# Kernel tuning notes

Hardware: AMD Instinct MI355X
Metric: run time of the kernel (lower is better)

Reference implementation:

```python
import jax, jax.numpy as jnp
import numpy as np

EMBED = 1024
HEADS = 16
HEAD_DIM = EMBED // HEADS
B, S = 4, 2048


def setup_inputs() -> dict:
    key = jax.random.key(0)
    ks = jax.random.split(key, 8)
    values = jax.random.normal(ks[0], (B, S, EMBED), dtype=jnp.float32)
    keys_in = jax.random.normal(ks[1], (B, S, EMBED), dtype=jnp.float32)
    query = jax.random.normal(ks[2], (B, S, EMBED), dtype=jnp.float32)
    mask = jnp.ones((B, 1, 1, S), dtype=jnp.int32)
    sc = 1.0 / np.sqrt(HEAD_DIM)
    Wv = jax.random.normal(ks[3], (HEAD_DIM, HEAD_DIM), dtype=jnp.float32) * sc
    Wk = jax.random.normal(ks[4], (HEAD_DIM, HEAD_DIM), dtype=jnp.float32) * sc
    Wq = jax.random.normal(ks[5], (HEAD_DIM, HEAD_DIM), dtype=jnp.float32) * sc
    Wo = jax.random.normal(ks[6], (EMBED, EMBED), dtype=jnp.float32) * (1.0 / np.sqrt(EMBED))
    bo = jnp.zeros((EMBED,), dtype=jnp.float32)
    return {"values": values, "keys": keys_in, "query": query, "mask": mask,
            "Wv": Wv, "Wk": Wk, "Wq": Wq, "Wo": Wo, "bo": bo}


def reference(values, keys, query, mask, Wv, Wk, Wq, Wo, bo):
    n = query.shape[0]
    vl, kl, ql = values.shape[1], keys.shape[1], query.shape[1]
    h, d = HEADS, HEAD_DIM
    # split heads: [n, len, h, d]
    v = values.reshape(n, vl, h, d)
    k = keys.reshape(n, kl, h, d)
    q = query.reshape(n, ql, h, d)
    # per-head linear projections (torch Linear: x @ W.T), shared across heads
    v = jnp.einsum('nlhd,ed->nlhe', v, Wv)
    k = jnp.einsum('nlhd,ed->nlhe', k, Wk)
    q = jnp.einsum('nlhd,ed->nlhe', q, Wq)
    # attention scores [n, h, q, k]
    energy = jnp.einsum('nqhd,nkhd->nhqk', q, k)
    energy = jnp.where(mask == 0, jnp.float32(-1e20), energy)
    # NOTE: original scales by sqrt(embed_size), not sqrt(head_dim)
    attn = jax.nn.softmax(energy / jnp.sqrt(jnp.float32(EMBED)), axis=3)
    out = jnp.einsum('nhql,nlhd->nqhd', attn, v).reshape(n, ql, h * d)
    return out @ Wo.T + bo
```

## Files before the change

### kernel.cpp

```cpp
#include <hip/hip_runtime.h>
#include <hip/hip_bf16.h>


#define SS 2048
#define HH 16
#define DD 64

typedef __attribute__((ext_vector_type(8))) short bf16x8;
typedef __attribute__((ext_vector_type(4))) short s16x4;
typedef __attribute__((ext_vector_type(4))) float f32x4;
typedef __attribute__((ext_vector_type(16))) float f32x16;

__device__ __forceinline__ short f2bf(float f) {
  union { float f; unsigned u; } c; c.f = f;
  unsigned r = (c.u + 0x7FFFu + ((c.u >> 16) & 1u)) >> 16;
  return (short)r;
}

__device__ __forceinline__ int cvtpk(float lo, float hi) {
  int r;
  asm("v_cvt_pk_bf16_f32 %0, %1, %2" : "=v"(r) : "v"(lo), "v"(hi));
  return r;
}

__device__ __forceinline__ float fexp2(float x) {
  float r;
  asm("v_exp_f32 %0, %1" : "=v"(r) : "v"(x));
  return r;
}

__global__ __launch_bounds__(256) void proj_kernel(
    const float* __restrict__ xq, const float* __restrict__ xk, const float* __restrict__ xv,
    const float* __restrict__ Wq, const float* __restrict__ Wk, const float* __restrict__ Wv,
    short* __restrict__ qp, short* __restrict__ kp, short* __restrict__ vp)
{
  __shared__ short xlds[128][72];
  __shared__ short wlds[3][64][72];
  const int t = threadIdx.x;
  const int lane = t & 63;
  const int w = t >> 6;
  const int l15 = lane & 15, l4 = lane >> 4;

  const float* wsrc[3] = {Wq, Wk, Wv};
#pragma unroll
  for (int z = 0; z < 3; ++z) {
#pragma unroll
    for (int i = 0; i < 4; ++i) {
      int fi = (t + i * 256) * 4;
      int row = fi >> 6, col = fi & 63;
      float4 a = *(const float4*)(wsrc[z] + fi);
      s16x4 sv = { f2bf(a.x), f2bf(a.y), f2bf(a.z), f2bf(a.w) };
      *(s16x4*)&wlds[z][row][col] = sv;
    }
  }

  const long r0 = (long)blockIdx.x * 128;
  const float* xin[3] = {xq, xk, xv};
  short* outp[3] = {qp, kp, vp};
  const float SCQ = 0.03125f * 1.4426950408889634f;

#pragma unroll
  for (int z = 0; z < 3; ++z) {
    __syncthreads();
    const float* src = xin[z] + r0 * 64;
#pragma unroll
    for (int i = 0; i < 8; ++i) {
      int fi = (t + i * 256) * 4;
      int row = fi >> 6, col = fi & 63;
      float4 a = *(const float4*)(src + fi);
      s16x4 sv = { f2bf(a.x), f2bf(a.y), f2bf(a.z), f2bf(a.w) };
      *(s16x4*)&xlds[row][col] = sv;
    }
    __syncthreads();

    bf16x8 af[2][2];
#pragma unroll
    for (int mi = 0; mi < 2; ++mi)
#pragma unroll
      for (int kb = 0; kb < 2; ++kb)
        af[mi][kb] = *(const bf16x8*)&xlds[w * 32 + mi * 16 + l15][kb * 32 + l4 * 8];

    f32x4 acc[2][4];
#pragma unroll
    for (int mi = 0; mi < 2; ++mi)
#pragma unroll
      for (int nt = 0; nt < 4; ++nt)
        acc[mi][nt] = (f32x4){0.f, 0.f, 0.f, 0.f};

#pragma unroll
    for (int nt = 0; nt < 4; ++nt)
#pragma unroll
      for (int kb = 0; kb < 2; ++kb) {
        bf16x8 bfr = *(const bf16x8*)&wlds[z][nt * 16 + l15][kb * 32 + l4 * 8];
#pragma unroll
        for (int mi = 0; mi < 2; ++mi)
          acc[mi][nt] = __builtin_amdgcn_mfma_f32_16x16x32_bf16(af[mi][kb], bfr, acc[mi][nt], 0, 0, 0);
      }

    short* dst = outp[z];
    const float sc = (z == 0) ? SCQ : 1.0f;
#pragma unroll
    for (int mi = 0; mi < 2; ++mi)
#pragma unroll
      for (int nt = 0; nt < 4; ++nt)
#pragma unroll
        for (int j = 0; j < 4; ++j) {
          int r = (int)r0 + w * 32 + mi * 16 + l4 * 4 + j;
          int e = nt * 16 + l15;
          int h = r & 15, bs = r >> 4;
          int b = bs >> 11, s = bs & 2047;
          dst[(((long)(b * 16 + h) * 2048 + s) << 6) + e] = f2bf(acc[mi][nt][j] * sc);
        }
  }
}

__global__ __launch_bounds__(256) void wo_cvt(const float* __restrict__ Wo,
                                              short* __restrict__ wob) {
  long i = ((long)blockIdx.x * 256 + threadIdx.x) * 4;
  float4 a = *(const float4*)(Wo + i);
  s16x4 sv = { f2bf(a.x), f2bf(a.y), f2bf(a.z), f2bf(a.w) };
  *(s16x4*)(wob + i) = sv;
}

__global__ __launch_bounds__(256) void vt_kernel(const short* __restrict__ vp,
                                                 short* __restrict__ vpt) {
  __shared__ short tl[64][72];
  const int t = threadIdx.x;
  const long base_in = (long)blockIdx.y * SS * DD + (long)blockIdx.x * 64 * DD;
#pragma unroll
  for (int i = 0; i < 2; ++i) {
    int c = t + i * 256;
    int s = c >> 3, d0 = (c & 7) * 8;
    bf16x8 v = *(const bf16x8*)(vp + base_in + s * 64 + d0);
#pragma unroll
    for (int j = 0; j < 8; ++j) tl[d0 + j][s] = v[j];
  }
  __syncthreads();
  const long base_out = (long)blockIdx.y * DD * SS + (long)blockIdx.x * 64;
#pragma unroll
  for (int i = 0; i < 2; ++i) {
    int c = t + i * 256;
    int d = c >> 3, s0 = (c & 7) * 8;
    *(bf16x8*)(vpt + base_out + (long)d * SS + s0) = *(const bf16x8*)&tl[d][s0];
  }
}

__global__ __launch_bounds__(256, 4) void attn_kernel(
    const short* __restrict__ qp, const short* __restrict__ kp, const short* __restrict__ vpt,
    const int* __restrict__ mask, short* __restrict__ ao)
{
  __shared__ short klds[64][72];
  __shared__ short vtlds[64][72];
  __shared__ int tile_ok[32];
  const int t = threadIdx.x, lane = t & 63, w = t >> 6;
  const int l31 = lane & 31, hi = lane >> 5;
  const int wg = (blockIdx.x & 7) * 128 + (blockIdx.x >> 3);
  const int bh = wg >> 4, qt = wg & 15;
  const int b = bh >> 4, h = bh & 15;
  const short* qb  = qp + (long)bh * SS * DD;
  const short* kbp = kp + (long)bh * SS * DD;
  const short* vtp = vpt + (long)bh * DD * SS;
  const int* mb = mask + b * SS;

  if (t < 32) tile_ok[t] = 1;
  __syncthreads();
  {
    int ok = 1;
#pragma unroll
    for (int i = 0; i < 8; ++i) ok &= (mb[t * 8 + i] != 0);
    if (!ok) tile_ok[t >> 3] = 0;
  }

  const int q = qt * 128 + w * 32 + l31;
  bf16x8 qf[4];
#pragma unroll
  for (int dblk = 0; dblk < 4; ++dblk)
    qf[dblk] = *(const bf16x8*)(qb + (long)q * 64 + dblk * 16 + hi * 8);

  const int sr = t >> 2;
  const int sc = (t & 3) * 16;
  const int v5 = sr & 31;
  const int prow = (sr & 32) + (v5 & 3) + 4 * ((v5 >> 3) & 1)
                 + 8 * (2 * ((v5 >> 4) & 1) + ((v5 >> 2) & 1));
  const short* kr_ptr = kbp + (long)sr * 64 + sc;
  const short* vr_ptr = vtp + (long)sr * SS + sc;

  bf16x8 kr0 = *(const bf16x8*)(kr_ptr);
  bf16x8 kr1 = *(const bf16x8*)(kr_ptr + 8);
  bf16x8 vr0 = *(const bf16x8*)(vr_ptr);
  bf16x8 vr1 = *(const bf16x8*)(vr_ptr + 8);

  const f32x16 fzero = {0.f,0.f,0.f,0.f,0.f,0.f,0.f,0.f,
                        0.f,0.f,0.f,0.f,0.f,0.f,0.f,0.f};
  f32x16 oacc[2];
  oacc[0] = fzero; oacc[1] = fzero;
  float l_reg = 0.f;

  for (int kt = 0; kt < SS / 64; ++kt) {
    const int k0 = kt * 64;
    __syncthreads();
    *(bf16x8*)&klds[prow][sc]      = kr0;
    *(bf16x8*)&klds[prow][sc + 8]  = kr1;
    *(bf16x8*)&vtlds[sr][sc]       = vr0;
    *(bf16x8*)&vtlds[sr][sc + 8]   = vr1;
    __syncthreads();
    {
      const int k0n = (kt < 31) ? k0 + 64 : k0;
      kr0 = *(const bf16x8*)(kr_ptr + (long)k0n * 64);
      kr1 = *(const bf16x8*)(kr_ptr + (long)k0n * 64 + 8);
      vr0 = *(const bf16x8*)(vr_ptr + k0n);
      vr1 = *(const bf16x8*)(vr_ptr + k0n + 8);
    }

    f32x16 sacc[2];
    __builtin_amdgcn_s_setprio(1);
#pragma unroll
    for (int kb = 0; kb < 2; ++kb) {
      bf16x8 ka0 = *(const bf16x8*)&klds[kb * 32 + l31][hi * 8];
      sacc[kb] = __builtin_amdgcn_mfma_f32_32x32x16_bf16(ka0, qf[0], fzero, 0, 0, 0);
#pragma unroll
      for (int dblk = 1; dblk < 4; ++dblk) {
        bf16x8 ka = *(const bf16x8*)&klds[kb * 32 + l31][dblk * 16 + hi * 8];
        sacc[kb] = __builtin_amdgcn_mfma_f32_32x32x16_bf16(ka, qf[dblk], sacc[kb], 0, 0, 0);
      }
    }
    __builtin_amdgcn_s_setprio(0);

    if (!tile_ok[kt]) {
#pragma unroll
      for (int kb = 0; kb < 2; ++kb)
#pragma unroll
        for (int r = 0; r < 16; ++r) {
          int kv = k0 + kb * 32 + 16 * ((r >> 3) & 1) + 8 * hi
                 + 4 * ((r >> 2) & 1) + (r & 3);
          if (mb[kv] == 0) sacc[kb][r] = -1e30f;
        }
    }

    float s0 = 0.f, s1 = 0.f, s2 = 0.f, s3 = 0.f;
#pragma unroll
    for (int kb = 0; kb < 2; ++kb)
#pragma unroll
      for (int r = 0; r < 16; r += 4) {
        float p0 = fexp2(sacc[kb][r]);
        float p1 = fexp2(sacc[kb][r + 1]);
        float p2 = fexp2(sacc[kb][r + 2]);
        float p3 = fexp2(sacc[kb][r + 3]);
        sacc[kb][r] = p0; sacc[kb][r + 1] = p1;
        sacc[kb][r + 2] = p2; sacc[kb][r + 3] = p3;
        s0 += p0; s1 += p1; s2 += p2; s3 += p3;
      }
    float sum = (s0 + s1) + (s2 + s3);
    sum += __shfl_xor(sum, 32);
    l_reg += sum;

    union PW { int wd[4]; bf16x8 v; } pa[4];
#pragma unroll
    for (int kb = 0; kb < 2; ++kb)
#pragma unroll
      for (int s1i = 0; s1i < 2; ++s1i)
#pragma unroll
        for (int w2 = 0; w2 < 4; ++w2)
          pa[kb * 2 + s1i].wd[w2] =
              cvtpk(sacc[kb][8 * s1i + 2 * w2], sacc[kb][8 * s1i + 2 * w2 + 1]);

    __builtin_amdgcn_s_setprio(1);
#pragma unroll
    for (int dt = 0; dt < 2; ++dt)
#pragma unroll
      for (int ks = 0; ks < 4; ++ks) {
        bf16x8 va = *(const bf16x8*)&vtlds[dt * 32 + l31][ks * 16 + hi * 8];
        oacc[dt] = __builtin_amdgcn_mfma_f32_32x32x16_bf16(va, pa[ks].v, oacc[dt], 0, 0, 0);
      }
    __builtin_amdgcn_s_setprio(0);
  }

  float inv = 1.f / l_reg;
#pragma unroll
  for (int dt = 0; dt < 2; ++dt)
#pragma unroll
    for (int g = 0; g < 4; ++g) {
      s16x4 sv;
#pragma unroll
      for (int j = 0; j < 4; ++j) sv[j] = f2bf(oacc[dt][g * 4 + j] * inv);
      int d0 = dt * 32 + g * 8 + hi * 4;
      *(s16x4*)(ao + (long)(b * SS + q) * 1024 + h * 64 + d0) = sv;
    }
}

__global__ __launch_bounds__(256) void out_gemm(
    const short* __restrict__ ao, const short* __restrict__ wob,
    const float* __restrict__ bo, float* __restrict__ out)
{
  __shared__ short alds[128][72];
  __shared__ short blds[128][72];
  const int t = threadIdx.x, lane = t & 63, w = t >> 6;
  const int l15 = lane & 15, l4 = lane >> 4;
  const int wm = w >> 1, wn = w & 1;
  const long m0 = (long)blockIdx.y * 128;
  const int n0 = blockIdx.x * 128;

  f32x4 acc[4][4];
#pragma unroll
  for (int mi = 0; mi < 4; ++mi)
#pragma unroll
    for (int ni = 0; ni < 4; ++ni) acc[mi][ni] = (f32x4){0.f, 0.f, 0.f, 0.f};

  for (int k0 = 0; k0 < 1024; k0 += 64) {
    __syncthreads();
#pragma unroll
    for (int i = 0; i < 4; ++i) {
      int f = t * 8 + i * 2048;
      int row = f >> 6, col = f & 63;
      *(bf16x8*)&alds[row][col] = *(const bf16x8*)(ao + (m0 + row) * 1024 + k0 + col);
      *(bf16x8*)&blds[row][col] = *(const bf16x8*)(wob + (long)(n0 + row) * 1024 + k0 + col);
    }
    __syncthreads();
#pragma unroll
    for (int kb = 0; kb < 2; ++kb) {
      bf16x8 af[4], bfr[4];
#pragma unroll
      for (int mi = 0; mi < 4; ++mi)
        af[mi] = *(const bf16x8*)&alds[wm * 64 + mi * 16 + l15][kb * 32 + l4 * 8];
#pragma unroll
      for (int ni = 0; ni < 4; ++ni)
        bfr[ni] = *(const bf16x8*)&blds[wn * 64 + ni * 16 + l15][kb * 32 + l4 * 8];
#pragma unroll
      for (int mi = 0; mi < 4; ++mi)
#pragma unroll
        for (int ni = 0; ni < 4; ++ni)
          acc[mi][ni] = __builtin_amdgcn_mfma_f32_16x16x32_bf16(af[mi], bfr[ni], acc[mi][ni], 0, 0, 0);
    }
  }
#pragma unroll
  for (int ni = 0; ni < 4; ++ni) {
    float bias = bo[n0 + wn * 64 + ni * 16 + l15];
#pragma unroll
    for (int mi = 0; mi < 4; ++mi)
#pragma unroll
      for (int j = 0; j < 4; ++j)
        out[(m0 + wm * 64 + mi * 16 + l4 * 4 + j) * 1024 + n0 + wn * 64 + ni * 16 + l15] =
            acc[mi][ni][j] + bias;
  }
}

extern "C" void kernel_launch(void* const* d_in, const int* in_sizes, int n_in,
                              void* d_out, int out_size, void* d_ws, size_t ws_size,
                              hipStream_t stream) {
  const float* values = (const float*)d_in[0];
  const float* keys   = (const float*)d_in[1];
  const float* query  = (const float*)d_in[2];
  const int*   mask   = (const int*)d_in[3];
  const float* Wv     = (const float*)d_in[4];
  const float* Wk     = (const float*)d_in[5];
  const float* Wq     = (const float*)d_in[6];
  const float* Wo     = (const float*)d_in[7];
  const float* bo     = (const float*)d_in[8];
  float* out = (float*)d_out;

  const long NTOK = 4L * SS * HH * DD;
  short* qp  = (short*)d_ws;
  short* kp  = qp + NTOK;
  short* vp  = kp + NTOK;
  short* aot = vp + NTOK;
  short* wob = aot + NTOK;
  short* vpt = wob + 1024 * 1024;

  hipLaunchKernelGGL(proj_kernel, dim3(1024), dim3(256), 0, stream,
                     query, keys, values, Wq, Wk, Wv, qp, kp, vp);
  hipLaunchKernelGGL(wo_cvt, dim3(1024), dim3(256), 0, stream, Wo, wob);
  hipLaunchKernelGGL(vt_kernel, dim3(32, 64), dim3(256), 0, stream, vp, vpt);
  hipLaunchKernelGGL(attn_kernel, dim3(1024), dim3(256), 0, stream,
                     qp, kp, vpt, mask, aot);
  hipLaunchKernelGGL(out_gemm, dim3(8, 64), dim3(256), 0, stream,
                     aot, wob, bo, out);
}
```

Baseline: 151.1 us.

## Double-buffer LDS tiles in attention and output GEMM with one barrier per step

Both the attention kernel and the output-projection GEMM now use ping-pong LDS buffers. Each iteration writes the prefetched next tile into the alternate buffer while computing on the current one, so only one __syncthreads per step remains and global prefetch runs two tiles ahead. This targets barrier stalls and load latency in the inner loops. In exchange it doubles LDS use per block, which may lower occupancy, and keeps more prefetch registers live.

```diff
diff --git a/kernel.cpp b/kernel.cpp
--- a/kernel.cpp
+++ b/kernel.cpp
@@ -149,8 +149,8 @@
     const short* __restrict__ qp, const short* __restrict__ kp, const short* __restrict__ vpt,
     const int* __restrict__ mask, short* __restrict__ ao)
 {
-  __shared__ short klds[64][72];
-  __shared__ short vtlds[64][72];
+  __shared__ short klds[2][64][72];
+  __shared__ short vtlds[2][64][72];
   __shared__ int tile_ok[32];
   const int t = threadIdx.x, lane = t & 63, w = t >> 6;
   const int l31 = lane & 31, hi = lane >> 5;
@@ -189,6 +189,14 @@
   bf16x8 kr1 = *(const bf16x8*)(kr_ptr + 8);
   bf16x8 vr0 = *(const bf16x8*)(vr_ptr);
   bf16x8 vr1 = *(const bf16x8*)(vr_ptr + 8);
+  *(bf16x8*)&klds[0][prow][sc]      = kr0;
+  *(bf16x8*)&klds[0][prow][sc + 8]  = kr1;
+  *(bf16x8*)&vtlds[0][sr][sc]       = vr0;
+  *(bf16x8*)&vtlds[0][sr][sc + 8]   = vr1;
+  kr0 = *(const bf16x8*)(kr_ptr + 64 * 64);
+  kr1 = *(const bf16x8*)(kr_ptr + 64 * 64 + 8);
+  vr0 = *(const bf16x8*)(vr_ptr + 64);
+  vr1 = *(const bf16x8*)(vr_ptr + 64 + 8);
 
   const f32x16 fzero = {0.f,0.f,0.f,0.f,0.f,0.f,0.f,0.f,
                         0.f,0.f,0.f,0.f,0.f,0.f,0.f,0.f};
@@ -197,30 +205,23 @@
   float l_reg = 0.f;
 
   for (int kt = 0; kt < SS / 64; ++kt) {
+    const int cur = kt & 1, nxt = cur ^ 1;
     const int k0 = kt * 64;
     __syncthreads();
-    *(bf16x8*)&klds[prow][sc]      = kr0;
-    *(bf16x8*)&klds[prow][sc + 8]  = kr1;
-    *(bf16x8*)&vtlds[sr][sc]       = vr0;
-    *(bf16x8*)&vtlds[sr][sc + 8]   = vr1;
-    __syncthreads();
-    {
-      const int k0n = (kt < 31) ? k0 + 64 : k0;
-      kr0 = *(const bf16x8*)(kr_ptr + (long)k0n * 64);
-      kr1 = *(const bf16x8*)(kr_ptr + (long)k0n * 64 + 8);
-      vr0 = *(const bf16x8*)(vr_ptr + k0n);
-      vr1 = *(const bf16x8*)(vr_ptr + k0n + 8);
-    }
+    *(bf16x8*)&klds[nxt][prow][sc]      = kr0;
+    *(bf16x8*)&klds[nxt][prow][sc + 8]  = kr1;
+    *(bf16x8*)&vtlds[nxt][sr][sc]       = vr0;
+    *(bf16x8*)&vtlds[nxt][sr][sc + 8]   = vr1;
 
     f32x16 sacc[2];
     __builtin_amdgcn_s_setprio(1);
 #pragma unroll
     for (int kb = 0; kb < 2; ++kb) {
-      bf16x8 ka0 = *(const bf16x8*)&klds[kb * 32 + l31][hi * 8];
+      bf16x8 ka0 = *(const bf16x8*)&klds[cur][kb * 32 + l31][hi * 8];
       sacc[kb] = __builtin_amdgcn_mfma_f32_32x32x16_bf16(ka0, qf[0], fzero, 0, 0, 0);
 #pragma unroll
       for (int dblk = 1; dblk < 4; ++dblk) {
-        bf16x8 ka = *(const bf16x8*)&klds[kb * 32 + l31][dblk * 16 + hi * 8];
+        bf16x8 ka = *(const bf16x8*)&klds[cur][kb * 32 + l31][dblk * 16 + hi * 8];
         sacc[kb] = __builtin_amdgcn_mfma_f32_32x32x16_bf16(ka, qf[dblk], sacc[kb], 0, 0, 0);
       }
     }
@@ -269,10 +270,19 @@
     for (int dt = 0; dt < 2; ++dt)
 #pragma unroll
       for (int ks = 0; ks < 4; ++ks) {
-        bf16x8 va = *(const bf16x8*)&vtlds[dt * 32 + l31][ks * 16 + hi * 8];
+        bf16x8 va = *(const bf16x8*)&vtlds[cur][dt * 32 + l31][ks * 16 + hi * 8];
         oacc[dt] = __builtin_amdgcn_mfma_f32_32x32x16_bf16(va, pa[ks].v, oacc[dt], 0, 0, 0);
       }
     __builtin_amdgcn_s_setprio(0);
+
+    {
+      const int ktn = (kt < 30) ? kt + 2 : 31;
+      const long k0n = (long)ktn * 64;
+      kr0 = *(const bf16x8*)(kr_ptr + k0n * 64);
+      kr1 = *(const bf16x8*)(kr_ptr + k0n * 64 + 8);
+      vr0 = *(const bf16x8*)(vr_ptr + k0n);
+      vr1 = *(const bf16x8*)(vr_ptr + k0n + 8);
+    }
   }
 
   float inv = 1.f / l_reg;
@@ -292,44 +302,75 @@
     const short* __restrict__ ao, const short* __restrict__ wob,
     const float* __restrict__ bo, float* __restrict__ out)
 {
-  __shared__ short alds[128][72];
-  __shared__ short blds[128][72];
+  __shared__ short alds[2][128][72];
+  __shared__ short blds[2][128][72];
   const int t = threadIdx.x, lane = t & 63, w = t >> 6;
   const int l15 = lane & 15, l4 = lane >> 4;
   const int wm = w >> 1, wn = w & 1;
   const long m0 = (long)blockIdx.y * 128;
   const int n0 = blockIdx.x * 128;
 
+  const int srow = t >> 3;
+  const int scol = (t & 7) * 8;
+
   f32x4 acc[4][4];
 #pragma unroll
   for (int mi = 0; mi < 4; ++mi)
 #pragma unroll
     for (int ni = 0; ni < 4; ++ni) acc[mi][ni] = (f32x4){0.f, 0.f, 0.f, 0.f};
 
-  for (int k0 = 0; k0 < 1024; k0 += 64) {
+  bf16x8 ar[4], br[4];
+#pragma unroll
+  for (int i = 0; i < 4; ++i) {
+    int row = srow + i * 32;
+    ar[i] = *(const bf16x8*)(ao + (m0 + row) * 1024 + scol);
+    br[i] = *(const bf16x8*)(wob + (long)(n0 + row) * 1024 + scol);
+  }
+#pragma unroll
+  for (int i = 0; i < 4; ++i) {
+    int row = srow + i * 32;
+    *(bf16x8*)&alds[0][row][scol] = ar[i];
+    *(bf16x8*)&blds[0][row][scol] = br[i];
+  }
+#pragma unroll
+  for (int i = 0; i < 4; ++i) {
+    int row = srow + i * 32;
+    ar[i] = *(const bf16x8*)(ao + (m0 + row) * 1024 + 64 + scol);
+    br[i] = *(const bf16x8*)(wob + (long)(n0 + row) * 1024 + 64 + scol);
+  }
+
+  for (int ki = 0; ki < 16; ++ki) {
+    const int cur = ki & 1, nxt = cur ^ 1;
     __syncthreads();
 #pragma unroll
     for (int i = 0; i < 4; ++i) {
-      int f = t * 8 + i * 2048;
-      int row = f >> 6, col = f & 63;
-      *(bf16x8*)&alds[row][col] = *(const bf16x8*)(ao + (m0 + row) * 1024 + k0 + col);
-      *(bf16x8*)&blds[row][col] = *(const bf16x8*)(wob + (long)(n0 + row) * 1024 + k0 + col);
-    }
-    __syncthreads();
+      int row = srow + i * 32;
+      *(bf16x8*)&alds[nxt][row][scol] = ar[i];
+      *(bf16x8*)&blds[nxt][row][scol] = br[i];
+    }
 #pragma unroll
     for (int kb = 0; kb < 2; ++kb) {
       bf16x8 af[4], bfr[4];
 #pragma unroll
       for (int mi = 0; mi < 4; ++mi)
-        af[mi] = *(const bf16x8*)&alds[wm * 64 + mi * 16 + l15][kb * 32 + l4 * 8];
+        af[mi] = *(const bf16x8*)&alds[cur][wm * 64 + mi * 16 + l15][kb * 32 + l4 * 8];
 #pragma unroll
       for (int ni = 0; ni < 4; ++ni)
-        bfr[ni] = *(const bf16x8*)&blds[wn * 64 + ni * 16 + l15][kb * 32 + l4 * 8];
+        bfr[ni] = *(const bf16x8*)&blds[cur][wn * 64 + ni * 16 + l15][kb * 32 + l4 * 8];
 #pragma unroll
       for (int mi = 0; mi < 4; ++mi)
 #pragma unroll
         for (int ni = 0; ni < 4; ++ni)
           acc[mi][ni] = __builtin_amdgcn_mfma_f32_16x16x32_bf16(af[mi], bfr[ni], acc[mi][ni], 0, 0, 0);
+    }
+    {
+      const int kn = ((ki < 14) ? ki + 2 : 15) * 64;
+#pragma unroll
+      for (int i = 0; i < 4; ++i) {
+        int row = srow + i * 32;
+        ar[i] = *(const bf16x8*)(ao + (m0 + row) * 1024 + kn + scol);
+        br[i] = *(const bf16x8*)(wob + (long)(n0 + row) * 1024 + kn + scol);
+      }
     }
   }
 #pragma unroll
```

After: 143.2 us. 5.3% less time.
